# Optimization experiments

Hardware: AMD Instinct MI355X
Metric: run time of the kernel (lower is better)

Reference implementation:

```python
import jax, jax.numpy as jnp
import numpy as np

NUM_USERS = 1_000_000
NUM_ITEMS = 1_000_000
EMB_DIM = 64
HIDDEN = 128
BATCH = 16384


def setup_inputs() -> dict:
    key = jax.random.key(0)
    ks = jax.random.split(key, 8)
    users = jax.random.randint(ks[0], (BATCH,), 0, NUM_USERS)
    items = jax.random.randint(ks[1], (BATCH,), 0, NUM_ITEMS)
    user_emb = 0.01 * jax.random.normal(ks[2], (NUM_USERS, EMB_DIM), dtype=jnp.float32)
    item_emb = 0.01 * jax.random.normal(ks[3], (NUM_ITEMS, EMB_DIM), dtype=jnp.float32)
    user_bias = jnp.zeros((NUM_USERS, 1), dtype=jnp.float32)
    item_bias = jnp.zeros((NUM_ITEMS, 1), dtype=jnp.float32)
    global_bias = jnp.zeros((1,), dtype=jnp.float32)
    # xavier_uniform for Linear layers
    lim1 = float(np.sqrt(6.0 / (2 * EMB_DIM + HIDDEN)))
    w1 = jax.random.uniform(ks[4], (HIDDEN, 2 * EMB_DIM), minval=-lim1, maxval=lim1, dtype=jnp.float32)
    b1 = jnp.zeros((HIDDEN,), dtype=jnp.float32)
    lim2 = float(np.sqrt(6.0 / (HIDDEN + 1)))
    w2 = jax.random.uniform(ks[5], (1, HIDDEN), minval=-lim2, maxval=lim2, dtype=jnp.float32)
    b2 = jnp.zeros((1,), dtype=jnp.float32)
    return {
        "users": users, "items": items,
        "user_emb": user_emb, "item_emb": item_emb,
        "user_bias": user_bias, "item_bias": item_bias,
        "global_bias": global_bias,
        "w1": w1, "b1": b1, "w2": w2, "b2": b2,
    }


def reference(users, items, user_emb, item_emb, user_bias, item_bias,
              global_bias, w1, b1, w2, b2):
    user_vecs = user_emb[users]            # [B, D]
    item_vecs = item_emb[items]            # [B, D]
    dot = jnp.sum(user_vecs * item_vecs, axis=1)  # [B]
    mlp_in = jnp.concatenate([user_vecs, item_vecs], axis=1)  # [B, 2D]
    h = jax.nn.relu(mlp_in @ w1.T + b1)    # [B, H]
    mlp_score = (h @ w2.T + b2)[:, 0]      # [B]
    scores = (dot
              + user_bias[users][:, 0]
              + item_bias[items][:, 0]
              + global_bias
              + mlp_score)
    return scores
```

## Files before the change

### kernel.cpp

```cpp
#include <hip/hip_runtime.h>

#define BLOCK 256
#define EPB 32
#define LDK 136

typedef __attribute__((ext_vector_type(8))) short short8;
typedef __attribute__((ext_vector_type(4))) float f32x4;

__device__ __forceinline__ unsigned short f2bf(float f) {
    unsigned u = __float_as_uint(f);
    u += 0x7FFF + ((u >> 16) & 1);
    return (unsigned short)(u >> 16);
}

__global__ __launch_bounds__(BLOCK, 2) void mf_fused(
    const int* __restrict__ users, const int* __restrict__ items,
    const float* __restrict__ user_emb, const float* __restrict__ item_emb,
    const float* __restrict__ user_bias, const float* __restrict__ item_bias,
    const float* __restrict__ global_bias,
    const float* __restrict__ w1, const float* __restrict__ b1,
    const float* __restrict__ w2, const float* __restrict__ b2,
    float* __restrict__ out)
{
    __shared__ unsigned short sA[EPB * LDK];
    __shared__ unsigned short sB[128 * LDK];
    __shared__ float sSum[EPB];
    __shared__ float sP[2][EPB];
    __shared__ float sB1[128];
    __shared__ float sW2[128];

    const int tid = threadIdx.x;
    const int e0 = blockIdx.x * EPB;

    const int c  = tid & 15;
    const int er = tid >> 4;
    const int uid_a = users[e0 + er];
    const int uid_b = users[e0 + er + 16];
    const int iid_a = items[e0 + er];
    const int iid_b = items[e0 + er + 16];

    if (tid < 128) { sB1[tid] = b1[tid]; sW2[tid] = w2[tid]; }

    {
        const int c2 = tid & 31;
        const int h0 = tid >> 5;
        #pragma unroll
        for (int it = 0; it < 16; ++it) {
            const int h = h0 + it * 8;
            const float4 wv = *(const float4*)(w1 + h * 128 + c2 * 4);
            ushort4 pk;
            pk.x = f2bf(wv.x); pk.y = f2bf(wv.y); pk.z = f2bf(wv.z); pk.w = f2bf(wv.w);
            *(ushort4*)&sB[h * LDK + c2 * 4] = pk;
        }
    }

    {
        const float4 ua = *(const float4*)(user_emb + (size_t)uid_a * 64 + c * 4);
        const float4 va = *(const float4*)(item_emb + (size_t)iid_a * 64 + c * 4);
        const float4 ub = *(const float4*)(user_emb + (size_t)uid_b * 64 + c * 4);
        const float4 vb = *(const float4*)(item_emb + (size_t)iid_b * 64 + c * 4);
        const float gb = global_bias[0] + b2[0];
        const float uba = user_bias[uid_a], ubb = user_bias[uid_b];
        const float iba = item_bias[iid_a], ibb = item_bias[iid_b];

        ushort4 pk;
        pk.x = f2bf(ua.x); pk.y = f2bf(ua.y); pk.z = f2bf(ua.z); pk.w = f2bf(ua.w);
        *(ushort4*)&sA[er * LDK + c * 4] = pk;
        pk.x = f2bf(va.x); pk.y = f2bf(va.y); pk.z = f2bf(va.z); pk.w = f2bf(va.w);
        *(ushort4*)&sA[er * LDK + 64 + c * 4] = pk;
        pk.x = f2bf(ub.x); pk.y = f2bf(ub.y); pk.z = f2bf(ub.z); pk.w = f2bf(ub.w);
        *(ushort4*)&sA[(er + 16) * LDK + c * 4] = pk;
        pk.x = f2bf(vb.x); pk.y = f2bf(vb.y); pk.z = f2bf(vb.z); pk.w = f2bf(vb.w);
        *(ushort4*)&sA[(er + 16) * LDK + 64 + c * 4] = pk;

        float pa = ua.x * va.x + ua.y * va.y + ua.z * va.z + ua.w * va.w;
        float pb = ub.x * vb.x + ub.y * vb.y + ub.z * vb.z + ub.w * vb.w;
        #define RED16(p) { p += __shfl_xor(p, 1); p += __shfl_xor(p, 2); \
                           p += __shfl_xor(p, 4); p += __shfl_xor(p, 8); }
        RED16(pa) RED16(pb)
        if (c == 0) {
            sSum[er]      = pa + uba + iba + gb;
            sSum[er + 16] = pb + ubb + ibb + gb;
        }
    }

    __syncthreads();

    const int lane  = tid & 63;
    const int wv    = tid >> 6;
    const int quad  = lane >> 4;
    const int nidx  = lane & 15;
    const int mrow0 = (wv & 1) * 16;
    const int nhalf = wv >> 1;
    const int hbase = nhalf * 64;

    f32x4 acc[4];
    #pragma unroll
    for (int nt = 0; nt < 4; ++nt) acc[nt] = (f32x4){0.f, 0.f, 0.f, 0.f};

    #pragma unroll
    for (int kk = 0; kk < 4; ++kk) {
        const short8 a = *(const short8*)&sA[(mrow0 + nidx) * LDK + kk * 32 + quad * 8];
        #pragma unroll
        for (int nt = 0; nt < 4; ++nt) {
            const short8 b = *(const short8*)&sB[(hbase + nt * 16 + nidx) * LDK + kk * 32 + quad * 8];
            acc[nt] = __builtin_amdgcn_mfma_f32_16x16x32_bf16(a, b, acc[nt], 0, 0, 0);
        }
    }

    float p0 = 0.f, p1 = 0.f, p2 = 0.f, p3 = 0.f;
    #pragma unroll
    for (int nt = 0; nt < 4; ++nt) {
        const int h = hbase + nt * 16 + nidx;
        const float b1v = sB1[h];
        const float w2v = sW2[h];
        p0 += fmaxf(acc[nt][0] + b1v, 0.f) * w2v;
        p1 += fmaxf(acc[nt][1] + b1v, 0.f) * w2v;
        p2 += fmaxf(acc[nt][2] + b1v, 0.f) * w2v;
        p3 += fmaxf(acc[nt][3] + b1v, 0.f) * w2v;
    }
    RED16(p0) RED16(p1) RED16(p2) RED16(p3)

    if (nidx == 0) {
        const int eb = mrow0 + quad * 4;
        sP[nhalf][eb + 0] = p0;
        sP[nhalf][eb + 1] = p1;
        sP[nhalf][eb + 2] = p2;
        sP[nhalf][eb + 3] = p3;
    }
    __syncthreads();

    if (tid < EPB)
        out[e0 + tid] = sSum[tid] + sP[0][tid] + sP[1][tid];
}

extern "C" void kernel_launch(void* const* d_in, const int* in_sizes, int n_in,
                              void* d_out, int out_size, void* d_ws, size_t ws_size,
                              hipStream_t stream) {
    const int*   users       = (const int*)d_in[0];
    const int*   items       = (const int*)d_in[1];
    const float* user_emb    = (const float*)d_in[2];
    const float* item_emb    = (const float*)d_in[3];
    const float* user_bias   = (const float*)d_in[4];
    const float* item_bias   = (const float*)d_in[5];
    const float* global_bias = (const float*)d_in[6];
    const float* w1          = (const float*)d_in[7];
    const float* b1          = (const float*)d_in[8];
    const float* w2          = (const float*)d_in[9];
    const float* b2          = (const float*)d_in[10];
    float* out = (float*)d_out;

    const int batch = in_sizes[0];
    const int grid = batch / EPB;
    mf_fused<<<grid, BLOCK, 0, stream>>>(users, items, user_emb, item_emb,
        user_bias, item_bias, global_bias, w1, b1, w2, b2, out);
}
```

Before: 400.4 us.

## Quadruple block threads so each thread gathers one embedding slice and each wave one tile

Grows the block from 256 to 1024 threads while keeping 32 elements per block. Each thread now loads a single float4 of user or item embedding, and the dot product pairs halves via a cross-lane shuffle. Each wave computes one 16x16 MFMA output tile instead of four, and the partial MLP sums are reduced across 8 slots. The aim is more waves and memory requests in flight to hide random-gather latency, at the cost of an extra barrier, index staging through shared memory and lower per-thread work.

```diff
diff --git a/kernel.cpp b/kernel.cpp
--- a/kernel.cpp
+++ b/kernel.cpp
@@ -1,6 +1,6 @@
 #include <hip/hip_runtime.h>
 
-#define BLOCK 256
+#define BLOCK 1024
 #define EPB 32
 #define LDK 136
 
@@ -13,7 +13,10 @@
     return (unsigned short)(u >> 16);
 }
 
-__global__ __launch_bounds__(BLOCK, 2) void mf_fused(
+#define RED16(p) { p += __shfl_xor(p, 1); p += __shfl_xor(p, 2); \
+                   p += __shfl_xor(p, 4); p += __shfl_xor(p, 8); }
+
+__global__ __launch_bounds__(BLOCK, 8) void mf_fused(
     const int* __restrict__ users, const int* __restrict__ items,
     const float* __restrict__ user_emb, const float* __restrict__ item_emb,
     const float* __restrict__ user_bias, const float* __restrict__ item_bias,
@@ -24,29 +27,26 @@
 {
     __shared__ unsigned short sA[EPB * LDK];
     __shared__ unsigned short sB[128 * LDK];
-    __shared__ float sSum[EPB];
-    __shared__ float sP[2][EPB];
+    __shared__ int   sUid[EPB], sIid[EPB];
+    __shared__ float sBias[EPB];
+    __shared__ float sDot[EPB];
+    __shared__ float sP[8][EPB];
     __shared__ float sB1[128];
     __shared__ float sW2[128];
 
     const int tid = threadIdx.x;
     const int e0 = blockIdx.x * EPB;
 
-    const int c  = tid & 15;
-    const int er = tid >> 4;
-    const int uid_a = users[e0 + er];
-    const int uid_b = users[e0 + er + 16];
-    const int iid_a = items[e0 + er];
-    const int iid_b = items[e0 + er + 16];
-
+    int uid = 0, iid = 0;
+    if (tid < EPB) { uid = users[e0 + tid]; iid = items[e0 + tid]; }
     if (tid < 128) { sB1[tid] = b1[tid]; sW2[tid] = w2[tid]; }
 
     {
         const int c2 = tid & 31;
         const int h0 = tid >> 5;
         #pragma unroll
-        for (int it = 0; it < 16; ++it) {
-            const int h = h0 + it * 8;
+        for (int it = 0; it < 4; ++it) {
+            const int h = h0 + it * 32;
             const float4 wv = *(const float4*)(w1 + h * 128 + c2 * 4);
             ushort4 pk;
             pk.x = f2bf(wv.x); pk.y = f2bf(wv.y); pk.z = f2bf(wv.z); pk.w = f2bf(wv.w);
@@ -54,84 +54,76 @@
         }
     }
 
+    if (tid < EPB) { sUid[tid] = uid; sIid[tid] = iid; }
+    __syncthreads();
+
     {
-        const float4 ua = *(const float4*)(user_emb + (size_t)uid_a * 64 + c * 4);
-        const float4 va = *(const float4*)(item_emb + (size_t)iid_a * 64 + c * 4);
-        const float4 ub = *(const float4*)(user_emb + (size_t)uid_b * 64 + c * 4);
-        const float4 vb = *(const float4*)(item_emb + (size_t)iid_b * 64 + c * 4);
-        const float gb = global_bias[0] + b2[0];
-        const float uba = user_bias[uid_a], ubb = user_bias[uid_b];
-        const float iba = item_bias[iid_a], ibb = item_bias[iid_b];
+        const int el   = tid >> 5;
+        const int half = (tid >> 4) & 1;
+        const int c    = tid & 15;
+        const int idx  = half ? sIid[el] : sUid[el];
+        const float* base = half ? item_emb : user_emb;
+        const float4 a = *(const float4*)(base + (size_t)idx * 64 + c * 4);
 
         ushort4 pk;
-        pk.x = f2bf(ua.x); pk.y = f2bf(ua.y); pk.z = f2bf(ua.z); pk.w = f2bf(ua.w);
-        *(ushort4*)&sA[er * LDK + c * 4] = pk;
-        pk.x = f2bf(va.x); pk.y = f2bf(va.y); pk.z = f2bf(va.z); pk.w = f2bf(va.w);
-        *(ushort4*)&sA[er * LDK + 64 + c * 4] = pk;
-        pk.x = f2bf(ub.x); pk.y = f2bf(ub.y); pk.z = f2bf(ub.z); pk.w = f2bf(ub.w);
-        *(ushort4*)&sA[(er + 16) * LDK + c * 4] = pk;
-        pk.x = f2bf(vb.x); pk.y = f2bf(vb.y); pk.z = f2bf(vb.z); pk.w = f2bf(vb.w);
-        *(ushort4*)&sA[(er + 16) * LDK + 64 + c * 4] = pk;
+        pk.x = f2bf(a.x); pk.y = f2bf(a.y); pk.z = f2bf(a.z); pk.w = f2bf(a.w);
+        *(ushort4*)&sA[el * LDK + half * 64 + c * 4] = pk;
 
-        float pa = ua.x * va.x + ua.y * va.y + ua.z * va.z + ua.w * va.w;
-        float pb = ub.x * vb.x + ub.y * vb.y + ub.z * vb.z + ub.w * vb.w;
-        #define RED16(p) { p += __shfl_xor(p, 1); p += __shfl_xor(p, 2); \
-                           p += __shfl_xor(p, 4); p += __shfl_xor(p, 8); }
-        RED16(pa) RED16(pb)
-        if (c == 0) {
-            sSum[er]      = pa + uba + iba + gb;
-            sSum[er + 16] = pb + ubb + ibb + gb;
-        }
+        float4 o;
+        o.x = __shfl_xor(a.x, 16); o.y = __shfl_xor(a.y, 16);
+        o.z = __shfl_xor(a.z, 16); o.w = __shfl_xor(a.w, 16);
+        float p = a.x * o.x + a.y * o.y + a.z * o.z + a.w * o.w;
+        RED16(p)
+        if ((tid & 31) == 0) sDot[el] = p;
     }
 
+    if (tid < EPB) {
+        const float gb = global_bias[0] + b2[0];
+        sBias[tid] = user_bias[uid] + item_bias[iid] + gb;
+    }
     __syncthreads();
 
     const int lane  = tid & 63;
-    const int wv    = tid >> 6;
+    const int wvid  = tid >> 6;
     const int quad  = lane >> 4;
     const int nidx  = lane & 15;
-    const int mrow0 = (wv & 1) * 16;
-    const int nhalf = wv >> 1;
-    const int hbase = nhalf * 64;
+    const int mhalf = wvid & 1;
+    const int n8    = wvid >> 1;
+    const int hb    = n8 * 16;
 
-    f32x4 acc[4];
-    #pragma unroll
-    for (int nt = 0; nt < 4; ++nt) acc[nt] = (f32x4){0.f, 0.f, 0.f, 0.f};
-
+    f32x4 acc = (f32x4){0.f, 0.f, 0.f, 0.f};
     #pragma unroll
     for (int kk = 0; kk < 4; ++kk) {
-        const short8 a = *(const short8*)&sA[(mrow0 + nidx) * LDK + kk * 32 + quad * 8];
-        #pragma unroll
-        for (int nt = 0; nt < 4; ++nt) {
-            const short8 b = *(const short8*)&sB[(hbase + nt * 16 + nidx) * LDK + kk * 32 + quad * 8];
-            acc[nt] = __builtin_amdgcn_mfma_f32_16x16x32_bf16(a, b, acc[nt], 0, 0, 0);
-        }
+        const short8 a = *(const short8*)&sA[(mhalf * 16 + nidx) * LDK + kk * 32 + quad * 8];
+        const short8 b = *(const short8*)&sB[(hb + nidx) * LDK + kk * 32 + quad * 8];
+        acc = __builtin_amdgcn_mfma_f32_16x16x32_bf16(a, b, acc, 0, 0, 0);
     }
 
-    float p0 = 0.f, p1 = 0.f, p2 = 0.f, p3 = 0.f;
-    #pragma unroll
-    for (int nt = 0; nt < 4; ++nt) {
-        const int h = hbase + nt * 16 + nidx;
+    {
+        const int h = hb + nidx;
         const float b1v = sB1[h];
         const float w2v = sW2[h];
-        p0 += fmaxf(acc[nt][0] + b1v, 0.f) * w2v;
-        p1 += fmaxf(acc[nt][1] + b1v, 0.f) * w2v;
-        p2 += fmaxf(acc[nt][2] + b1v, 0.f) * w2v;
-        p3 += fmaxf(acc[nt][3] + b1v, 0.f) * w2v;
-    }
-    RED16(p0) RED16(p1) RED16(p2) RED16(p3)
-
-    if (nidx == 0) {
-        const int eb = mrow0 + quad * 4;
-        sP[nhalf][eb + 0] = p0;
-        sP[nhalf][eb + 1] = p1;
-        sP[nhalf][eb + 2] = p2;
-        sP[nhalf][eb + 3] = p3;
+        float p0 = fmaxf(acc[0] + b1v, 0.f) * w2v;
+        float p1 = fmaxf(acc[1] + b1v, 0.f) * w2v;
+        float p2 = fmaxf(acc[2] + b1v, 0.f) * w2v;
+        float p3 = fmaxf(acc[3] + b1v, 0.f) * w2v;
+        RED16(p0) RED16(p1) RED16(p2) RED16(p3)
+        if (nidx == 0) {
+            const int eb = mhalf * 16 + quad * 4;
+            sP[n8][eb + 0] = p0;
+            sP[n8][eb + 1] = p1;
+            sP[n8][eb + 2] = p2;
+            sP[n8][eb + 3] = p3;
+        }
     }
     __syncthreads();
 
-    if (tid < EPB)
-        out[e0 + tid] = sSum[tid] + sP[0][tid] + sP[1][tid];
+    if (tid < EPB) {
+        float s = sDot[tid] + sBias[tid];
+        #pragma unroll
+        for (int k = 0; k < 8; ++k) s += sP[k][tid];
+        out[e0 + tid] = s;
+    }
 }
 
 extern "C" void kernel_launch(void* const* d_in, const int* in_sizes, int n_in,
```

After: 401.9 us. About the same (+0.4%).
